# Performance work log

Measured on AMD Instinct MI355X. Metric: run time of the kernel, lower is better.

Reference implementation:

```python
import jax, jax.numpy as jnp
import numpy as np
import math

BS, NPOS, D_IN = 8, 384, 512
H, D_OUT = 8, 512
DK = D_OUT // H  # 64


def setup_inputs() -> dict:
    key = jax.random.key(0)
    ks = jax.random.split(key, 13)
    s = 0.02
    return {
        "q": jax.random.normal(ks[0], (BS, NPOS, D_IN), jnp.float32),
        "k": jax.random.normal(ks[1], (BS, NPOS, D_IN), jnp.float32),
        "v": jax.random.normal(ks[2], (BS, NPOS, D_IN), jnp.float32),
        "rpos_k": jax.random.normal(ks[3], (NPOS, NPOS, H, DK), jnp.float32) * s,
        "rpos_v": jax.random.normal(ks[4], (NPOS, NPOS, H, DK), jnp.float32) * s,
        "Wq": jax.random.normal(ks[5], (D_IN, D_OUT), jnp.float32) * s,
        "bq": jnp.zeros((D_OUT,), jnp.float32),
        "Wk": jax.random.normal(ks[6], (D_IN, D_OUT), jnp.float32) * s,
        "bk": jnp.zeros((D_OUT,), jnp.float32),
        "Wv": jax.random.normal(ks[7], (D_IN, D_OUT), jnp.float32) * s,
        "bv": jnp.zeros((D_OUT,), jnp.float32),
        "Wo": jax.random.normal(ks[8], (D_OUT, D_OUT), jnp.float32) * s,
        "bo": jnp.zeros((D_OUT,), jnp.float32),
    }


def reference(q, k, v, rpos_k, rpos_v, Wq, bq, Wk, bk, Wv, bv, Wo, bo):
    # model_name = 'with_pe' path; mask=None; dropout in eval mode (no-op)
    bs = q.shape[0]
    inv_sqrt_dk = 1.0 / math.sqrt(DK)

    qh = (q @ Wq + bq).reshape(bs, -1, H, DK).transpose(0, 2, 1, 3)  # bs,h,n,dk
    kh = (k @ Wk + bk).reshape(bs, -1, H, DK).transpose(0, 2, 1, 3)
    original_v = v @ Wv + bv                                          # bs,n,d_out
    vh = original_v.reshape(bs, -1, H, DK).transpose(0, 2, 1, 3)

    # standard content-content scores
    std_scores = jnp.einsum('bhnd,bhmd->bhnm', qh, kh) * inv_sqrt_dk
    # relative-position scores: q_n . rpos_k[n, m, h] -- computed inline,
    # no bs-broadcast materialization of rpos_k
    pos_scores = jnp.einsum('bhnd,nmhd->bhnm', qh, rpos_k) * inv_sqrt_dk

    scores = jax.nn.softmax(std_scores + pos_scores, axis=-1)
    # NOTE: original code divides the attention output by sqrt(d_k) again
    attn_out = jnp.einsum('bhnm,bhmd->bhnd', scores, vh) * inv_sqrt_dk

    concat = attn_out.transpose(0, 2, 1, 3).reshape(bs, -1, D_OUT)
    output = concat @ Wo + bo
    return (original_v, output)
```

## Files before the change

### kernel.cpp

```cpp
#include <hip/hip_runtime.h>

#define NPOS 384
#define DMODEL 512
#define NH 8
#define DK 64
#define BS 8
#define MROWS (BS * NPOS)
#define SROW (NPOS * NPOS)

typedef __attribute__((ext_vector_type(8))) short bf16x8;
typedef __attribute__((ext_vector_type(4))) float f32x4;

__device__ __forceinline__ unsigned short f2bf(float x) {
  unsigned int u = __float_as_uint(x);
  return (unsigned short)((u + 0x7fffu + ((u >> 16) & 1u)) >> 16);
}
__device__ __forceinline__ unsigned int pk2(float lo, float hi) {
  unsigned int ul = __float_as_uint(lo), uh = __float_as_uint(hi);
  ul = (ul + 0x7fffu + ((ul >> 16) & 1u)) >> 16;
  uh = (uh + 0x7fffu + ((uh >> 16) & 1u)) & 0xffff0000u;
  return ul | uh;
}
__device__ __forceinline__ bf16x8 pack8(float4 a, float4 b) {
  union { uint4 u; bf16x8 v; } cv;
  cv.u = make_uint4(pk2(a.x, a.y), pk2(a.z, a.w), pk2(b.x, b.y), pk2(b.z, b.w));
  return cv.v;
}

__global__ __launch_bounds__(256) void convert_w(
    const float* __restrict__ Wq, const float* __restrict__ Wk,
    const float* __restrict__ Wv, const float* __restrict__ Wo,
    unsigned short* __restrict__ wt) {
  __shared__ float s[64][68];
  const int z = blockIdx.z;
  const float* W = z == 0 ? Wq : z == 1 ? Wk : z == 2 ? Wv : Wo;
  unsigned short* out = wt + (size_t)z * DMODEL * DMODEL;
  const int k0 = blockIdx.x * 64, n0 = blockIdx.y * 64;
  const int t = threadIdx.x;
#pragma unroll
  for (int i = 0; i < 4; ++i) {
    int f = t + i * 256;
    int kr = f >> 4, q4 = f & 15;
    *(float4*)&s[kr][q4 * 4] = *(const float4*)&W[(size_t)(k0 + kr) * DMODEL + n0 + q4 * 4];
  }
  __syncthreads();
#pragma unroll
  for (int i = 0; i < 2; ++i) {
    int slot = t + i * 256;
    int n = slot >> 3, kq = slot & 7;
    unsigned int p[4];
#pragma unroll
    for (int j = 0; j < 4; ++j)
      p[j] = pk2(s[kq * 8 + j * 2][n], s[kq * 8 + j * 2 + 1][n]);
    *(uint4*)&out[(size_t)(n0 + n) * DMODEL + k0 + kq * 8] = make_uint4(p[0], p[1], p[2], p[3]);
  }
}

__global__ __launch_bounds__(256) void convert_in(
    const float* __restrict__ qin, const float* __restrict__ kin,
    const float* __restrict__ vin, unsigned short* __restrict__ qkvb) {
  const int z = blockIdx.y;
  const float* src = z == 0 ? qin : z == 1 ? kin : vin;
  unsigned short* dst = qkvb + (size_t)z * MROWS * DMODEL;
  const size_t i = ((size_t)blockIdx.x * 256 + threadIdx.x) * 8;
  float4 a = *(const float4*)&src[i];
  float4 b = *(const float4*)&src[i + 4];
  union { uint4 u; bf16x8 v; } cv;
  cv.u = make_uint4(pk2(a.x, a.y), pk2(a.z, a.w), pk2(b.x, b.y), pk2(b.z, b.w));
  *(uint4*)&dst[i] = cv.u;
}

__global__ __launch_bounds__(256) void proj_qkv(
    const unsigned short* __restrict__ qkvb,
    const unsigned short* __restrict__ wt,
    const float* __restrict__ bq, const float* __restrict__ bk, const float* __restrict__ bv,
    unsigned short* __restrict__ qhb, unsigned short* __restrict__ khb,
    float* __restrict__ origv, unsigned short* __restrict__ vhT) {
  __shared__ unsigned short As[64][72];
  __shared__ unsigned short Bs[64][72];
  const int z = blockIdx.z;
  const unsigned short* A = qkvb + (size_t)z * MROWS * DMODEL;
  const unsigned short* Wt = wt + (size_t)z * DMODEL * DMODEL;
  const float* bias = z == 0 ? bq : z == 1 ? bk : bv;
  const int m0 = blockIdx.x * 64, n0 = blockIdx.y * 64;
  const int t = threadIdx.x, lane = t & 63, w = t >> 6;
  const int wr = w >> 1, wc = w & 1;
  const int l15 = lane & 15, l4 = lane >> 4;
  f32x4 acc[2][2] = {};
  for (int kt = 0; kt < 8; ++kt) {
    const int k0 = kt * 64;
#pragma unroll
    for (int i = 0; i < 2; ++i) {
      int s = t + i * 256;
      int row = s >> 3, kq = s & 7;
      *(uint4*)&As[row][kq * 8] = *(const uint4*)&A[(size_t)(m0 + row) * DMODEL + k0 + kq * 8];
      *(uint4*)&Bs[row][kq * 8] = *(const uint4*)&Wt[(size_t)(n0 + row) * DMODEL + k0 + kq * 8];
    }
    __syncthreads();
    bf16x8 af[2][2], bfr[2][2];
#pragma unroll
    for (int mf = 0; mf < 2; ++mf)
#pragma unroll
      for (int ks = 0; ks < 2; ++ks)
        af[mf][ks] = *(const bf16x8*)&As[wr * 32 + mf * 16 + l15][ks * 32 + l4 * 8];
#pragma unroll
    for (int nf = 0; nf < 2; ++nf)
#pragma unroll
      for (int ks = 0; ks < 2; ++ks)
        bfr[nf][ks] = *(const bf16x8*)&Bs[wc * 32 + nf * 16 + l15][ks * 32 + l4 * 8];
#pragma unroll
    for (int mf = 0; mf < 2; ++mf)
#pragma unroll
      for (int nf = 0; nf < 2; ++nf)
#pragma unroll
        for (int ks = 0; ks < 2; ++ks)
          acc[mf][nf] = __builtin_amdgcn_mfma_f32_16x16x32_bf16(af[mf][ks], bfr[nf][ks],
                                                                acc[mf][nf], 0, 0, 0);
    __syncthreads();
  }
#pragma unroll
  for (int mf = 0; mf < 2; ++mf)
#pragma unroll
    for (int nf = 0; nf < 2; ++nf) {
      const int row0 = m0 + wr * 32 + mf * 16 + l4 * 4;
      const int col = n0 + wc * 32 + nf * 16 + l15;
      const float bi = bias[col];
      if (z == 0) {
#pragma unroll
        for (int i = 0; i < 4; ++i)
          qhb[(size_t)(row0 + i) * DMODEL + col] = f2bf((acc[mf][nf][i] + bi) * 0.125f);
      } else if (z == 1) {
#pragma unroll
        for (int i = 0; i < 4; ++i)
          khb[(size_t)(row0 + i) * DMODEL + col] = f2bf(acc[mf][nf][i] + bi);
      } else {
        const int b = row0 / NPOS, n = row0 - b * NPOS;
        const int h = col >> 6, d = col & 63;
        float vals[4];
#pragma unroll
        for (int i = 0; i < 4; ++i) {
          vals[i] = acc[mf][nf][i] + bi;
          origv[(size_t)(row0 + i) * DMODEL + col] = vals[i];
        }
        ushort4 pk;
        pk.x = f2bf(vals[0]); pk.y = f2bf(vals[1]);
        pk.z = f2bf(vals[2]); pk.w = f2bf(vals[3]);
        *(ushort4*)&vhT[((size_t)((b * NH + h) * DK + d)) * NPOS + n] = pk;
      }
    }
}

__global__ __launch_bounds__(256) void scores_nt(
    const unsigned short* __restrict__ qhb, const unsigned short* __restrict__ khb,
    float* __restrict__ scores) {
  __shared__ unsigned short As[128][72];
  __shared__ unsigned short Bs[128][72];
  const int z = blockIdx.z, b = z >> 3, h = z & 7;
  const unsigned short* Ag = qhb + (size_t)b * NPOS * DMODEL + h * DK;
  const unsigned short* Bg = khb + (size_t)b * NPOS * DMODEL + h * DK;
  const int n0 = blockIdx.x * 128, m0 = blockIdx.y * 128;
  const int t = threadIdx.x, lane = t & 63, w = t >> 6;
  const int wr = w >> 1, wc = w & 1;
  const int l15 = lane & 15, l4 = lane >> 4;
#pragma unroll
  for (int i = 0; i < 4; ++i) {
    int s = t + i * 256;
    int row = s >> 3, kq = s & 7;
    *(uint4*)&As[row][kq * 8] = *(const uint4*)&Ag[(size_t)(n0 + row) * DMODEL + kq * 8];
    *(uint4*)&Bs[row][kq * 8] = *(const uint4*)&Bg[(size_t)(m0 + row) * DMODEL + kq * 8];
  }
  __syncthreads();
  f32x4 acc[4][4] = {};
  bf16x8 af[4][2], bfr[4][2];
#pragma unroll
  for (int mf = 0; mf < 4; ++mf)
#pragma unroll
    for (int ks = 0; ks < 2; ++ks)
      af[mf][ks] = *(const bf16x8*)&As[wr * 64 + mf * 16 + l15][ks * 32 + l4 * 8];
#pragma unroll
  for (int nf = 0; nf < 4; ++nf)
#pragma unroll
    for (int ks = 0; ks < 2; ++ks)
      bfr[nf][ks] = *(const bf16x8*)&Bs[wc * 64 + nf * 16 + l15][ks * 32 + l4 * 8];
#pragma unroll
  for (int mf = 0; mf < 4; ++mf)
#pragma unroll
    for (int nf = 0; nf < 4; ++nf)
#pragma unroll
      for (int ks = 0; ks < 2; ++ks)
        acc[mf][nf] = __builtin_amdgcn_mfma_f32_16x16x32_bf16(af[mf][ks], bfr[nf][ks],
                                                              acc[mf][nf], 0, 0, 0);
  float* C = scores + (size_t)z * SROW;
#pragma unroll
  for (int mf = 0; mf < 4; ++mf)
#pragma unroll
    for (int nf = 0; nf < 4; ++nf) {
      int rown = n0 + wr * 64 + mf * 16 + l4 * 4;
      int colm = m0 + wc * 64 + nf * 16 + l15;
#pragma unroll
      for (int i = 0; i < 4; ++i)
        C[(size_t)(rown + i) * NPOS + colm] = acc[mf][nf][i];
    }
}

__global__ __launch_bounds__(256) void pos_scores_mfma(
    const unsigned short* __restrict__ qhb,
    const float* __restrict__ rk,
    float* __restrict__ scores) {
  const int n = blockIdx.y;
  const int m0 = blockIdx.x * 16;
  const int t = threadIdx.x, lane = t & 63, w = t >> 6;
  const int l15 = lane & 15, l4 = lane >> 4;
  const int bcol = l15 & 7;
  const float* rkrow = rk + ((size_t)n * NPOS + m0 + l15) * (NH * DK);
  const unsigned short* qp = qhb + ((size_t)bcol * NPOS + n) * DMODEL;
#pragma unroll
  for (int hp = 0; hp < 2; ++hp) {
    const int h = w * 2 + hp;
    const int base = h * DK;
    f32x4 acc = {};
#pragma unroll
    for (int ks = 0; ks < 2; ++ks) {
      const int off = base + ks * 32 + l4 * 8;
      const float4 ra = *(const float4*)&rkrow[off];
      const float4 rb = *(const float4*)&rkrow[off + 4];
      bf16x8 af = pack8(ra, rb);
      bf16x8 bfr = *(const bf16x8*)&qp[off];
      acc = __builtin_amdgcn_mfma_f32_16x16x32_bf16(af, bfr, acc, 0, 0, 0);
    }
    if (l15 < 8) {
      float* srow = scores + ((size_t)(l15 * NH + h) * NPOS + n) * NPOS + m0 + l4 * 4;
      float4 c = *(float4*)srow;
      c.x += acc[0]; c.y += acc[1]; c.z += acc[2]; c.w += acc[3];
      *(float4*)srow = c;
    }
  }
}

__global__ __launch_bounds__(256) void softmax_bf(float* __restrict__ scores) {
  const int row = blockIdx.x * 4 + (threadIdx.x >> 6);
  const int lane = threadIdx.x & 63;
  float* s = scores + (size_t)row * NPOS;
  unsigned short* p = (unsigned short*)s;
  float v[6];
  float mx = -1e30f;
#pragma unroll
  for (int j = 0; j < 6; ++j) {
    v[j] = s[j * 64 + lane];
    mx = fmaxf(mx, v[j]);
  }
#pragma unroll
  for (int o = 32; o; o >>= 1) mx = fmaxf(mx, __shfl_xor(mx, o, 64));
  float sum = 0.f;
#pragma unroll
  for (int j = 0; j < 6; ++j) {
    v[j] = __expf(v[j] - mx);
    sum += v[j];
  }
#pragma unroll
  for (int o = 32; o; o >>= 1) sum += __shfl_xor(sum, o, 64);
  const float inv = 0.125f / sum;
#pragma unroll
  for (int j = 0; j < 6; ++j) p[j * 64 + lane] = f2bf(v[j] * inv);
}

__global__ __launch_bounds__(256) void pv_nt(
    const unsigned short* __restrict__ Pbase,
    const unsigned short* __restrict__ vhT,
    unsigned short* __restrict__ attb) {
  __shared__ unsigned short As[64][72];
  __shared__ unsigned short Bs[64][72];
  const int z = blockIdx.z, b = z >> 3, h = z & 7;
  const int n0 = blockIdx.x * 64;
  const unsigned short* Ag = Pbase + ((size_t)(z * NPOS + n0)) * 768;
  const unsigned short* Bg = vhT + (size_t)z * DK * NPOS;
  const int t = threadIdx.x, lane = t & 63, w = t >> 6;
  const int wr = w >> 1, wc = w & 1;
  const int l15 = lane & 15, l4 = lane >> 4;
  f32x4 acc[2][2] = {};
  for (int kt = 0; kt < 6; ++kt) {
    const int k0 = kt * 64;
#pragma unroll
    for (int i = 0; i < 2; ++i) {
      int s = t + i * 256;
      int row = s >> 3, kq = s & 7;
      *(uint4*)&As[row][kq * 8] = *(const uint4*)&Ag[(size_t)row * 768 + k0 + kq * 8];
      *(uint4*)&Bs[row][kq * 8] = *(const uint4*)&Bg[(size_t)row * NPOS + k0 + kq * 8];
    }
    __syncthreads();
    bf16x8 af[2][2], bfr[2][2];
#pragma unroll
    for (int mf = 0; mf < 2; ++mf)
#pragma unroll
      for (int ks = 0; ks < 2; ++ks)
        af[mf][ks] = *(const bf16x8*)&As[wr * 32 + mf * 16 + l15][ks * 32 + l4 * 8];
#pragma unroll
    for (int nf = 0; nf < 2; ++nf)
#pragma unroll
      for (int ks = 0; ks < 2; ++ks)
        bfr[nf][ks] = *(const bf16x8*)&Bs[wc * 32 + nf * 16 + l15][ks * 32 + l4 * 8];
#pragma unroll
    for (int mf = 0; mf < 2; ++mf)
#pragma unroll
      for (int nf = 0; nf < 2; ++nf)
#pragma unroll
        for (int ks = 0; ks < 2; ++ks)
          acc[mf][nf] = __builtin_amdgcn_mfma_f32_16x16x32_bf16(af[mf][ks], bfr[nf][ks],
                                                                acc[mf][nf], 0, 0, 0);
    __syncthreads();
  }
#pragma unroll
  for (int mf = 0; mf < 2; ++mf)
#pragma unroll
    for (int nf = 0; nf < 2; ++nf) {
      const int n = n0 + wr * 32 + mf * 16 + l4 * 4;
      const int d = wc * 32 + nf * 16 + l15;
#pragma unroll
      for (int i = 0; i < 4; ++i)
        attb[(size_t)(b * NPOS + n + i) * DMODEL + h * DK + d] = f2bf(acc[mf][nf][i]);
    }
}

__global__ __launch_bounds__(256) void proj_o(
    const unsigned short* __restrict__ attb, const unsigned short* __restrict__ WtO,
    const float* __restrict__ bo, float* __restrict__ outp) {
  __shared__ unsigned short As[64][72];
  __shared__ unsigned short Bs[64][72];
  const int m0 = blockIdx.x * 64, n0 = blockIdx.y * 64;
  const int t = threadIdx.x, lane = t & 63, w = t >> 6;
  const int wr = w >> 1, wc = w & 1;
  const int l15 = lane & 15, l4 = lane >> 4;
  f32x4 acc[2][2] = {};
  for (int kt = 0; kt < 8; ++kt) {
    const int k0 = kt * 64;
#pragma unroll
    for (int i = 0; i < 2; ++i) {
      int s = t + i * 256;
      int row = s >> 3, kq = s & 7;
      *(uint4*)&As[row][kq * 8] = *(const uint4*)&attb[(size_t)(m0 + row) * DMODEL + k0 + kq * 8];
      *(uint4*)&Bs[row][kq * 8] = *(const uint4*)&WtO[(size_t)(n0 + row) * DMODEL + k0 + kq * 8];
    }
    __syncthreads();
    bf16x8 af[2][2], bfr[2][2];
#pragma unroll
    for (int mf = 0; mf < 2; ++mf)
#pragma unroll
      for (int ks = 0; ks < 2; ++ks)
        af[mf][ks] = *(const bf16x8*)&As[wr * 32 + mf * 16 + l15][ks * 32 + l4 * 8];
#pragma unroll
    for (int nf = 0; nf < 2; ++nf)
#pragma unroll
      for (int ks = 0; ks < 2; ++ks)
        bfr[nf][ks] = *(const bf16x8*)&Bs[wc * 32 + nf * 16 + l15][ks * 32 + l4 * 8];
#pragma unroll
    for (int mf = 0; mf < 2; ++mf)
#pragma unroll
      for (int nf = 0; nf < 2; ++nf)
#pragma unroll
        for (int ks = 0; ks < 2; ++ks)
          acc[mf][nf] = __builtin_amdgcn_mfma_f32_16x16x32_bf16(af[mf][ks], bfr[nf][ks],
                                                                acc[mf][nf], 0, 0, 0);
    __syncthreads();
  }
#pragma unroll
  for (int mf = 0; mf < 2; ++mf)
#pragma unroll
    for (int nf = 0; nf < 2; ++nf) {
      const int row0 = m0 + wr * 32 + mf * 16 + l4 * 4;
      const int col = n0 + wc * 32 + nf * 16 + l15;
      const float bi = bo[col];
#pragma unroll
      for (int i = 0; i < 4; ++i)
        outp[(size_t)(row0 + i) * DMODEL + col] = acc[mf][nf][i] + bi;
    }
}

extern "C" void kernel_launch(void* const* d_in, const int* in_sizes, int n_in,
                              void* d_out, int out_size, void* d_ws, size_t ws_size,
                              hipStream_t stream) {
  const float* q  = (const float*)d_in[0];
  const float* k  = (const float*)d_in[1];
  const float* v  = (const float*)d_in[2];
  const float* rk = (const float*)d_in[3];
  const float* Wq = (const float*)d_in[5];
  const float* bq = (const float*)d_in[6];
  const float* Wk = (const float*)d_in[7];
  const float* bk = (const float*)d_in[8];
  const float* Wv = (const float*)d_in[9];
  const float* bv = (const float*)d_in[10];
  const float* Wo = (const float*)d_in[11];
  const float* bo = (const float*)d_in[12];

  const size_t TOK = (size_t)MROWS * DMODEL;
  unsigned short* wt   = (unsigned short*)d_ws;
  unsigned short* qhb  = wt + 4 * DMODEL * DMODEL;
  unsigned short* khb  = qhb + TOK;
  unsigned short* vhT  = khb + TOK;
  unsigned short* attb = vhT + TOK;
  float* scores = (float*)(attb + TOK);
  unsigned short* qkvb = (unsigned short*)scores;
  float* origv = (float*)d_out;
  float* outp = origv + TOK;

  dim3 blk(256);

  convert_w<<<dim3(8, 8, 4), blk, 0, stream>>>(Wq, Wk, Wv, Wo, wt);
  convert_in<<<dim3(768, 3), blk, 0, stream>>>(q, k, v, qkvb);
  proj_qkv<<<dim3(48, 8, 3), blk, 0, stream>>>(qkvb, wt, bq, bk, bv,
                                               qhb, khb, origv, vhT);
  scores_nt<<<dim3(3, 3, 64), blk, 0, stream>>>(qhb, khb, scores);
  pos_scores_mfma<<<dim3(24, 384), blk, 0, stream>>>(qhb, rk, scores);
  softmax_bf<<<dim3((BS * NH * NPOS) / 4), blk, 0, stream>>>(scores);
  pv_nt<<<dim3(6, 1, 64), blk, 0, stream>>>((const unsigned short*)scores, vhT, attb);
  proj_o<<<dim3(48, 8), blk, 0, stream>>>(attb, wt + 3 * DMODEL * DMODEL, bo, outp);
}
```

Before: 154.9 us.

## Fuse softmax into PV kernel, merge conversion kernels, enlarge projection GEMM tiles

Merges the input and weight conversion kernels into one launch. Moves the row softmax into the PV kernel, which keeps unnormalised bf16 probabilities in shared memory and applies 1/sum in the epilogue, so the scores no longer make an extra round trip through global memory. The QKV and output projection GEMMs move from 64x64 to 128x128 tiles for more reuse per block. The larger tiles cut the grid sizes, which risks lower occupancy and poor load balance on a GPU with many CUs.

```diff
diff --git a/kernel.cpp b/kernel.cpp
--- a/kernel.cpp
+++ b/kernel.cpp
@@ -27,16 +27,31 @@
   return cv.v;
 }
 
-__global__ __launch_bounds__(256) void convert_w(
+__global__ __launch_bounds__(256) void convert_all(
+    const float* __restrict__ qin, const float* __restrict__ kin,
+    const float* __restrict__ vin,
     const float* __restrict__ Wq, const float* __restrict__ Wk,
     const float* __restrict__ Wv, const float* __restrict__ Wo,
-    unsigned short* __restrict__ wt) {
+    unsigned short* __restrict__ qkvb, unsigned short* __restrict__ wt) {
+  const int z = blockIdx.y;
+  const int t = threadIdx.x;
+  if (z < 3) {
+    const float* src = z == 0 ? qin : z == 1 ? kin : vin;
+    unsigned short* dst = qkvb + (size_t)z * MROWS * DMODEL;
+    const size_t i = ((size_t)blockIdx.x * 256 + t) * 8;
+    float4 a = *(const float4*)&src[i];
+    float4 b = *(const float4*)&src[i + 4];
+    union { uint4 u; bf16x8 v; } cv;
+    cv.u = make_uint4(pk2(a.x, a.y), pk2(a.z, a.w), pk2(b.x, b.y), pk2(b.z, b.w));
+    *(uint4*)&dst[i] = cv.u;
+    return;
+  }
+  if (blockIdx.x >= 64) return;
   __shared__ float s[64][68];
-  const int z = blockIdx.z;
-  const float* W = z == 0 ? Wq : z == 1 ? Wk : z == 2 ? Wv : Wo;
-  unsigned short* out = wt + (size_t)z * DMODEL * DMODEL;
-  const int k0 = blockIdx.x * 64, n0 = blockIdx.y * 64;
-  const int t = threadIdx.x;
+  const int w = z - 3;
+  const float* W = w == 0 ? Wq : w == 1 ? Wk : w == 2 ? Wv : Wo;
+  unsigned short* out = wt + (size_t)w * DMODEL * DMODEL;
+  const int k0 = (blockIdx.x & 7) * 64, n0 = (blockIdx.x >> 3) * 64;
 #pragma unroll
   for (int i = 0; i < 4; ++i) {
     int f = t + i * 256;
@@ -54,20 +69,6 @@
       p[j] = pk2(s[kq * 8 + j * 2][n], s[kq * 8 + j * 2 + 1][n]);
     *(uint4*)&out[(size_t)(n0 + n) * DMODEL + k0 + kq * 8] = make_uint4(p[0], p[1], p[2], p[3]);
   }
-}
-
-__global__ __launch_bounds__(256) void convert_in(
-    const float* __restrict__ qin, const float* __restrict__ kin,
-    const float* __restrict__ vin, unsigned short* __restrict__ qkvb) {
-  const int z = blockIdx.y;
-  const float* src = z == 0 ? qin : z == 1 ? kin : vin;
-  unsigned short* dst = qkvb + (size_t)z * MROWS * DMODEL;
-  const size_t i = ((size_t)blockIdx.x * 256 + threadIdx.x) * 8;
-  float4 a = *(const float4*)&src[i];
-  float4 b = *(const float4*)&src[i + 4];
-  union { uint4 u; bf16x8 v; } cv;
-  cv.u = make_uint4(pk2(a.x, a.y), pk2(a.z, a.w), pk2(b.x, b.y), pk2(b.z, b.w));
-  *(uint4*)&dst[i] = cv.u;
 }
 
 __global__ __launch_bounds__(256) void proj_qkv(
@@ -76,42 +77,42 @@
     const float* __restrict__ bq, const float* __restrict__ bk, const float* __restrict__ bv,
     unsigned short* __restrict__ qhb, unsigned short* __restrict__ khb,
     float* __restrict__ origv, unsigned short* __restrict__ vhT) {
-  __shared__ unsigned short As[64][72];
-  __shared__ unsigned short Bs[64][72];
+  __shared__ unsigned short As[128][72];
+  __shared__ unsigned short Bs[128][72];
   const int z = blockIdx.z;
   const unsigned short* A = qkvb + (size_t)z * MROWS * DMODEL;
   const unsigned short* Wt = wt + (size_t)z * DMODEL * DMODEL;
   const float* bias = z == 0 ? bq : z == 1 ? bk : bv;
-  const int m0 = blockIdx.x * 64, n0 = blockIdx.y * 64;
+  const int m0 = blockIdx.x * 128, n0 = blockIdx.y * 128;
   const int t = threadIdx.x, lane = t & 63, w = t >> 6;
   const int wr = w >> 1, wc = w & 1;
   const int l15 = lane & 15, l4 = lane >> 4;
-  f32x4 acc[2][2] = {};
+  f32x4 acc[4][4] = {};
   for (int kt = 0; kt < 8; ++kt) {
     const int k0 = kt * 64;
 #pragma unroll
-    for (int i = 0; i < 2; ++i) {
+    for (int i = 0; i < 4; ++i) {
       int s = t + i * 256;
       int row = s >> 3, kq = s & 7;
       *(uint4*)&As[row][kq * 8] = *(const uint4*)&A[(size_t)(m0 + row) * DMODEL + k0 + kq * 8];
       *(uint4*)&Bs[row][kq * 8] = *(const uint4*)&Wt[(size_t)(n0 + row) * DMODEL + k0 + kq * 8];
     }
     __syncthreads();
-    bf16x8 af[2][2], bfr[2][2];
-#pragma unroll
-    for (int mf = 0; mf < 2; ++mf)
-#pragma unroll
-      for (int ks = 0; ks < 2; ++ks)
-        af[mf][ks] = *(const bf16x8*)&As[wr * 32 + mf * 16 + l15][ks * 32 + l4 * 8];
-#pragma unroll
-    for (int nf = 0; nf < 2; ++nf)
-#pragma unroll
-      for (int ks = 0; ks < 2; ++ks)
-        bfr[nf][ks] = *(const bf16x8*)&Bs[wc * 32 + nf * 16 + l15][ks * 32 + l4 * 8];
-#pragma unroll
-    for (int mf = 0; mf < 2; ++mf)
-#pragma unroll
-      for (int nf = 0; nf < 2; ++nf)
+    bf16x8 af[4][2], bfr[4][2];
+#pragma unroll
+    for (int mf = 0; mf < 4; ++mf)
+#pragma unroll
+      for (int ks = 0; ks < 2; ++ks)
+        af[mf][ks] = *(const bf16x8*)&As[wr * 64 + mf * 16 + l15][ks * 32 + l4 * 8];
+#pragma unroll
+    for (int nf = 0; nf < 4; ++nf)
+#pragma unroll
+      for (int ks = 0; ks < 2; ++ks)
+        bfr[nf][ks] = *(const bf16x8*)&Bs[wc * 64 + nf * 16 + l15][ks * 32 + l4 * 8];
+#pragma unroll
+    for (int mf = 0; mf < 4; ++mf)
+#pragma unroll
+      for (int nf = 0; nf < 4; ++nf)
 #pragma unroll
         for (int ks = 0; ks < 2; ++ks)
           acc[mf][nf] = __builtin_amdgcn_mfma_f32_16x16x32_bf16(af[mf][ks], bfr[nf][ks],
@@ -119,11 +120,11 @@
     __syncthreads();
   }
 #pragma unroll
-  for (int mf = 0; mf < 2; ++mf)
-#pragma unroll
-    for (int nf = 0; nf < 2; ++nf) {
-      const int row0 = m0 + wr * 32 + mf * 16 + l4 * 4;
-      const int col = n0 + wc * 32 + nf * 16 + l15;
+  for (int mf = 0; mf < 4; ++mf)
+#pragma unroll
+    for (int nf = 0; nf < 4; ++nf) {
+      const int row0 = m0 + wr * 64 + mf * 16 + l4 * 4;
+      const int col = n0 + wc * 64 + nf * 16 + l15;
       const float bi = bias[col];
       if (z == 0) {
 #pragma unroll
@@ -237,125 +238,125 @@
   }
 }
 
-__global__ __launch_bounds__(256) void softmax_bf(float* __restrict__ scores) {
-  const int row = blockIdx.x * 4 + (threadIdx.x >> 6);
-  const int lane = threadIdx.x & 63;
-  float* s = scores + (size_t)row * NPOS;
-  unsigned short* p = (unsigned short*)s;
-  float v[6];
-  float mx = -1e30f;
-#pragma unroll
-  for (int j = 0; j < 6; ++j) {
-    v[j] = s[j * 64 + lane];
-    mx = fmaxf(mx, v[j]);
-  }
-#pragma unroll
-  for (int o = 32; o; o >>= 1) mx = fmaxf(mx, __shfl_xor(mx, o, 64));
-  float sum = 0.f;
-#pragma unroll
-  for (int j = 0; j < 6; ++j) {
-    v[j] = __expf(v[j] - mx);
-    sum += v[j];
-  }
-#pragma unroll
-  for (int o = 32; o; o >>= 1) sum += __shfl_xor(sum, o, 64);
-  const float inv = 0.125f / sum;
-#pragma unroll
-  for (int j = 0; j < 6; ++j) p[j * 64 + lane] = f2bf(v[j] * inv);
-}
-
-__global__ __launch_bounds__(256) void pv_nt(
-    const unsigned short* __restrict__ Pbase,
+__global__ __launch_bounds__(256) void pv_sm(
+    const float* __restrict__ scores,
     const unsigned short* __restrict__ vhT,
     unsigned short* __restrict__ attb) {
-  __shared__ unsigned short As[64][72];
+  __shared__ unsigned short Ps[64][392];
   __shared__ unsigned short Bs[64][72];
-  const int z = blockIdx.z, b = z >> 3, h = z & 7;
+  __shared__ float invs[64];
+  const int z = blockIdx.y, b = z >> 3, h = z & 7;
   const int n0 = blockIdx.x * 64;
-  const unsigned short* Ag = Pbase + ((size_t)(z * NPOS + n0)) * 768;
+  const int t = threadIdx.x, lane = t & 63, w = t >> 6;
+  {
+    const int r = t >> 2, j = t & 3;
+    const float* srow = scores + ((size_t)z * NPOS + n0 + r) * NPOS;
+    float4 v[24];
+#pragma unroll
+    for (int i = 0; i < 24; ++i) v[i] = *(const float4*)&srow[i * 16 + j * 4];
+    float mx = -1e30f;
+#pragma unroll
+    for (int i = 0; i < 24; ++i)
+      mx = fmaxf(fmaxf(fmaxf(mx, v[i].x), fmaxf(v[i].y, v[i].z)), v[i].w);
+    mx = fmaxf(mx, __shfl_xor(mx, 1, 64));
+    mx = fmaxf(mx, __shfl_xor(mx, 2, 64));
+    float sum = 0.f;
+#pragma unroll
+    for (int i = 0; i < 24; ++i) {
+      v[i].x = __expf(v[i].x - mx); v[i].y = __expf(v[i].y - mx);
+      v[i].z = __expf(v[i].z - mx); v[i].w = __expf(v[i].w - mx);
+      sum += (v[i].x + v[i].y) + (v[i].z + v[i].w);
+    }
+    sum += __shfl_xor(sum, 1, 64);
+    sum += __shfl_xor(sum, 2, 64);
+    if (j == 0) invs[r] = 0.125f / sum;
+#pragma unroll
+    for (int i = 0; i < 24; ++i)
+      *(uint2*)&Ps[r][i * 16 + j * 4] = make_uint2(pk2(v[i].x, v[i].y), pk2(v[i].z, v[i].w));
+  }
+  __syncthreads();
+  const int wr = w >> 1, wc = w & 1;
+  const int l15 = lane & 15, l4 = lane >> 4;
   const unsigned short* Bg = vhT + (size_t)z * DK * NPOS;
+  f32x4 acc[2][2] = {};
+  for (int kt = 0; kt < 6; ++kt) {
+    const int k0 = kt * 64;
+#pragma unroll
+    for (int i = 0; i < 2; ++i) {
+      int s = t + i * 256;
+      int row = s >> 3, kq = s & 7;
+      *(uint4*)&Bs[row][kq * 8] = *(const uint4*)&Bg[(size_t)row * NPOS + k0 + kq * 8];
+    }
+    __syncthreads();
+    bf16x8 af[2][2], bfr[2][2];
+#pragma unroll
+    for (int mf = 0; mf < 2; ++mf)
+#pragma unroll
+      for (int ks = 0; ks < 2; ++ks)
+        af[mf][ks] = *(const bf16x8*)&Ps[wr * 32 + mf * 16 + l15][k0 + ks * 32 + l4 * 8];
+#pragma unroll
+    for (int nf = 0; nf < 2; ++nf)
+#pragma unroll
+      for (int ks = 0; ks < 2; ++ks)
+        bfr[nf][ks] = *(const bf16x8*)&Bs[wc * 32 + nf * 16 + l15][ks * 32 + l4 * 8];
+#pragma unroll
+    for (int mf = 0; mf < 2; ++mf)
+#pragma unroll
+      for (int nf = 0; nf < 2; ++nf)
+#pragma unroll
+        for (int ks = 0; ks < 2; ++ks)
+          acc[mf][nf] = __builtin_amdgcn_mfma_f32_16x16x32_bf16(af[mf][ks], bfr[nf][ks],
+                                                                acc[mf][nf], 0, 0, 0);
+    __syncthreads();
+  }
+#pragma unroll
+  for (int mf = 0; mf < 2; ++mf)
+#pragma unroll
+    for (int nf = 0; nf < 2; ++nf) {
+      const int nl = wr * 32 + mf * 16 + l4 * 4;
+      const int d = wc * 32 + nf * 16 + l15;
+#pragma unroll
+      for (int i = 0; i < 4; ++i)
+        attb[(size_t)(b * NPOS + n0 + nl + i) * DMODEL + h * DK + d] =
+            f2bf(acc[mf][nf][i] * invs[nl + i]);
+    }
+}
+
+__global__ __launch_bounds__(256) void proj_o(
+    const unsigned short* __restrict__ attb, const unsigned short* __restrict__ WtO,
+    const float* __restrict__ bo, float* __restrict__ outp) {
+  __shared__ unsigned short As[128][72];
+  __shared__ unsigned short Bs[128][72];
+  const int m0 = blockIdx.x * 128, n0 = blockIdx.y * 128;
   const int t = threadIdx.x, lane = t & 63, w = t >> 6;
   const int wr = w >> 1, wc = w & 1;
   const int l15 = lane & 15, l4 = lane >> 4;
-  f32x4 acc[2][2] = {};
-  for (int kt = 0; kt < 6; ++kt) {
-    const int k0 = kt * 64;
-#pragma unroll
-    for (int i = 0; i < 2; ++i) {
-      int s = t + i * 256;
-      int row = s >> 3, kq = s & 7;
-      *(uint4*)&As[row][kq * 8] = *(const uint4*)&Ag[(size_t)row * 768 + k0 + kq * 8];
-      *(uint4*)&Bs[row][kq * 8] = *(const uint4*)&Bg[(size_t)row * NPOS + k0 + kq * 8];
-    }
-    __syncthreads();
-    bf16x8 af[2][2], bfr[2][2];
-#pragma unroll
-    for (int mf = 0; mf < 2; ++mf)
-#pragma unroll
-      for (int ks = 0; ks < 2; ++ks)
-        af[mf][ks] = *(const bf16x8*)&As[wr * 32 + mf * 16 + l15][ks * 32 + l4 * 8];
-#pragma unroll
-    for (int nf = 0; nf < 2; ++nf)
-#pragma unroll
-      for (int ks = 0; ks < 2; ++ks)
-        bfr[nf][ks] = *(const bf16x8*)&Bs[wc * 32 + nf * 16 + l15][ks * 32 + l4 * 8];
-#pragma unroll
-    for (int mf = 0; mf < 2; ++mf)
-#pragma unroll
-      for (int nf = 0; nf < 2; ++nf)
-#pragma unroll
-        for (int ks = 0; ks < 2; ++ks)
-          acc[mf][nf] = __builtin_amdgcn_mfma_f32_16x16x32_bf16(af[mf][ks], bfr[nf][ks],
-                                                                acc[mf][nf], 0, 0, 0);
-    __syncthreads();
-  }
-#pragma unroll
-  for (int mf = 0; mf < 2; ++mf)
-#pragma unroll
-    for (int nf = 0; nf < 2; ++nf) {
-      const int n = n0 + wr * 32 + mf * 16 + l4 * 4;
-      const int d = wc * 32 + nf * 16 + l15;
-#pragma unroll
-      for (int i = 0; i < 4; ++i)
-        attb[(size_t)(b * NPOS + n + i) * DMODEL + h * DK + d] = f2bf(acc[mf][nf][i]);
-    }
-}
-
-__global__ __launch_bounds__(256) void proj_o(
-    const unsigned short* __restrict__ attb, const unsigned short* __restrict__ WtO,
-    const float* __restrict__ bo, float* __restrict__ outp) {
-  __shared__ unsigned short As[64][72];
-  __shared__ unsigned short Bs[64][72];
-  const int m0 = blockIdx.x * 64, n0 = blockIdx.y * 64;
-  const int t = threadIdx.x, lane = t & 63, w = t >> 6;
-  const int wr = w >> 1, wc = w & 1;
-  const int l15 = lane & 15, l4 = lane >> 4;
-  f32x4 acc[2][2] = {};
+  f32x4 acc[4][4] = {};
   for (int kt = 0; kt < 8; ++kt) {
     const int k0 = kt * 64;
 #pragma unroll
-    for (int i = 0; i < 2; ++i) {
+    for (int i = 0; i < 4; ++i) {
       int s = t + i * 256;
       int row = s >> 3, kq = s & 7;
       *(uint4*)&As[row][kq * 8] = *(const uint4*)&attb[(size_t)(m0 + row) * DMODEL + k0 + kq * 8];
       *(uint4*)&Bs[row][kq * 8] = *(const uint4*)&WtO[(size_t)(n0 + row) * DMODEL + k0 + kq * 8];
     }
     __syncthreads();
-    bf16x8 af[2][2], bfr[2][2];
-#pragma unroll
-    for (int mf = 0; mf < 2; ++mf)
-#pragma unroll
-      for (int ks = 0; ks < 2; ++ks)
-        af[mf][ks] = *(const bf16x8*)&As[wr * 32 + mf * 16 + l15][ks * 32 + l4 * 8];
-#pragma unroll
-    for (int nf = 0; nf < 2; ++nf)
-#pragma unroll
-      for (int ks = 0; ks < 2; ++ks)
-        bfr[nf][ks] = *(const bf16x8*)&Bs[wc * 32 + nf * 16 + l15][ks * 32 + l4 * 8];
-#pragma unroll
-    for (int mf = 0; mf < 2; ++mf)
-#pragma unroll
-      for (int nf = 0; nf < 2; ++nf)
+    bf16x8 af[4][2], bfr[4][2];
+#pragma unroll
+    for (int mf = 0; mf < 4; ++mf)
+#pragma unroll
+      for (int ks = 0; ks < 2; ++ks)
+        af[mf][ks] = *(const bf16x8*)&As[wr * 64 + mf * 16 + l15][ks * 32 + l4 * 8];
+#pragma unroll
+    for (int nf = 0; nf < 4; ++nf)
+#pragma unroll
+      for (int ks = 0; ks < 2; ++ks)
+        bfr[nf][ks] = *(const bf16x8*)&Bs[wc * 64 + nf * 16 + l15][ks * 32 + l4 * 8];
+#pragma unroll
+    for (int mf = 0; mf < 4; ++mf)
+#pragma unroll
+      for (int nf = 0; nf < 4; ++nf)
 #pragma unroll
         for (int ks = 0; ks < 2; ++ks)
           acc[mf][nf] = __builtin_amdgcn_mfma_f32_16x16x32_bf16(af[mf][ks], bfr[nf][ks],
@@ -363,11 +364,11 @@
     __syncthreads();
   }
 #pragma unroll
-  for (int mf = 0; mf < 2; ++mf)
-#pragma unroll
-    for (int nf = 0; nf < 2; ++nf) {
-      const int row0 = m0 + wr * 32 + mf * 16 + l4 * 4;
-      const int col = n0 + wc * 32 + nf * 16 + l15;
+  for (int mf = 0; mf < 4; ++mf)
+#pragma unroll
+    for (int nf = 0; nf < 4; ++nf) {
+      const int row0 = m0 + wr * 64 + mf * 16 + l4 * 4;
+      const int col = n0 + wc * 64 + nf * 16 + l15;
       const float bi = bo[col];
 #pragma unroll
       for (int i = 0; i < 4; ++i)
@@ -404,13 +405,11 @@
 
   dim3 blk(256);
 
-  convert_w<<<dim3(8, 8, 4), blk, 0, stream>>>(Wq, Wk, Wv, Wo, wt);
-  convert_in<<<dim3(768, 3), blk, 0, stream>>>(q, k, v, qkvb);
-  proj_qkv<<<dim3(48, 8, 3), blk, 0, stream>>>(qkvb, wt, bq, bk, bv,
+  convert_all<<<dim3(768, 7), blk, 0, stream>>>(q, k, v, Wq, Wk, Wv, Wo, qkvb, wt);
+  proj_qkv<<<dim3(24, 4, 3), blk, 0, stream>>>(qkvb, wt, bq, bk, bv,
                                                qhb, khb, origv, vhT);
   scores_nt<<<dim3(3, 3, 64), blk, 0, stream>>>(qhb, khb, scores);
   pos_scores_mfma<<<dim3(24, 384), blk, 0, stream>>>(qhb, rk, scores);
-  softmax_bf<<<dim3((BS * NH * NPOS) / 4), blk, 0, stream>>>(scores);
-  pv_nt<<<dim3(6, 1, 64), blk, 0, stream>>>((const unsigned short*)scores, vhT, attb);
-  proj_o<<<dim3(48, 8), blk, 0, stream>>>(attb, wt + 3 * DMODEL * DMODEL, bo, outp);
-}
+  pv_sm<<<dim3(6, 64), blk, 0, stream>>>(scores, vhT, attb);
+  proj_o<<<dim3(24, 4), blk, 0, stream>>>(attb, wt + 3 * DMODEL * DMODEL, bo, outp);
+}
```

Result: no change. 157.5 us (+1.7%).
